# Performance work log

Hardware: AMD Instinct MI355X
Metric: run time of the kernel (lower is better)

The kernel has to match this reference:

```python
import jax, jax.numpy as jnp
import numpy as np

B, S, S2, H, NH, DF, NL, NLAYER = 512, 6, 32, 256, 8, 2048, 3, 3
HD = H // NH


def _layernorm(x, g, b, eps=1e-5):
    mu = x.mean(-1, keepdims=True)
    var = ((x - mu) ** 2).mean(-1, keepdims=True)
    return (x - mu) / jnp.sqrt(var + eps) * g + b


def _pos_encoding(seq, d):
    pos = jnp.arange(seq, dtype=jnp.float32)[:, None]
    div = jnp.exp(jnp.arange(0, d, 2, dtype=jnp.float32) * (-jnp.log(10000.0) / d))
    ang = pos * div  # [seq, d/2]
    return jnp.stack([jnp.sin(ang), jnp.cos(ang)], axis=-1).reshape(seq, d)


def setup_inputs() -> dict:
    key = jax.random.key(0)
    ks = iter(jax.random.split(key, 40))
    sc = 0.02
    inp = {}
    inp['states'] = jax.random.normal(next(ks), (B, S, H), jnp.float32)
    inp['state_mask'] = jax.random.randint(next(ks), (B, S), 0, 2).astype(jnp.float32)
    inp['actions'] = jax.random.normal(next(ks), (B, S2, H), jnp.float32)
    inp['actions_mask'] = jnp.ones((B, S2), jnp.float32)
    # TransformerEncoder params (3 layers, stacked on leading axis)
    inp['Wqkv'] = jax.random.normal(next(ks), (NLAYER, 3 * H, H), jnp.float32) * sc
    inp['bqkv'] = jnp.zeros((NLAYER, 3 * H), jnp.float32)
    inp['Wo'] = jax.random.normal(next(ks), (NLAYER, H, H), jnp.float32) * sc
    inp['bo'] = jnp.zeros((NLAYER, H), jnp.float32)
    inp['ln1_g'] = jnp.ones((NLAYER, H), jnp.float32)
    inp['ln1_b'] = jnp.zeros((NLAYER, H), jnp.float32)
    inp['W1'] = jax.random.normal(next(ks), (NLAYER, DF, H), jnp.float32) * sc
    inp['b1'] = jnp.zeros((NLAYER, DF), jnp.float32)
    inp['W2'] = jax.random.normal(next(ks), (NLAYER, H, DF), jnp.float32) * sc
    inp['b2'] = jnp.zeros((NLAYER, H), jnp.float32)
    inp['ln2_g'] = jnp.ones((NLAYER, H), jnp.float32)
    inp['ln2_b'] = jnp.zeros((NLAYER, H), jnp.float32)
    # attn_layer MLP: Linear(2H->H), ReLU, Linear(H->1), ReLU
    inp['Wa1'] = jax.random.normal(next(ks), (H, 2 * H), jnp.float32) * sc
    inp['ba1'] = jnp.zeros((H,), jnp.float32)
    inp['Wa2'] = jax.random.normal(next(ks), (1, H), jnp.float32) * sc
    inp['ba2'] = jnp.zeros((1,), jnp.float32)
    # dueling value head
    inp['Wv'] = jax.random.normal(next(ks), (1, H), jnp.float32) * sc
    inp['bv'] = jnp.zeros((1,), jnp.float32)
    # per-label bilinear weight [num_labels, H, H] + bias
    inp['Wlab'] = jax.random.normal(next(ks), (NL, H, H), jnp.float32) * sc
    inp['blab'] = jax.random.normal(next(ks), (NL,), jnp.float32) * sc
    return inp


def _forward(states, state_mask, actions, actions_mask, Wqkv, bqkv, Wo, bo,
             ln1_g, ln1_b, W1, b1, W2, b2, ln2_g, ln2_b,
             Wa1, ba1, Wa2, ba2, Wv, bv, Wlab, blab):
    batch, seq, hs = states.shape
    seq2 = actions.shape[1]
    # positional encoding along seq axis (eval mode: dropout = identity)
    x = states + _pos_encoding(seq, hs)[None, :, :]
    # Faithful to original: [batch, seq, h] is fed to a seq-first torch
    # TransformerEncoder, so self-attention mixes across the BATCH axis (L=batch,
    # N=seq). Post-LN layers, relu FFN, dim_feedforward=2048.
    for i in range(NLAYER):
        L, N = x.shape[0], x.shape[1]
        qkv = jnp.einsum('lne,fe->lnf', x, Wqkv[i]) + bqkv[i]
        q, k, v = jnp.split(qkv, 3, axis=-1)
        q = q.reshape(L, N, NH, HD)
        k = k.reshape(L, N, NH, HD)
        v = v.reshape(L, N, NH, HD)
        scores = jnp.einsum('lnhd,mnhd->nhlm', q, k) / jnp.sqrt(jnp.float32(HD))
        attn = jax.nn.softmax(scores, axis=-1)
        ctx = jnp.einsum('nhlm,mnhd->lnhd', attn, v).reshape(L, N, hs)
        sa = jnp.einsum('lne,fe->lnf', ctx, Wo[i]) + bo[i]
        x = _layernorm(x + sa, ln1_g[i], ln1_b[i])
        hmid = jax.nn.relu(jnp.einsum('lne,fe->lnf', x, W1[i]) + b1[i])
        ff = jnp.einsum('lnf,ef->lne', hmid, W2[i]) + b2[i]
        x = _layernorm(x + ff, ln2_g[i], ln2_b[i])
    out = x  # [batch, seq, h]
    # --- attention_aggregate(actions, out, out, actions_mask, state_mask) ---
    mask = actions_mask[:, :, None] * state_mask[:, None, :]  # [B, seq2, seq]
    stack = jnp.concatenate([
        jnp.broadcast_to(actions[:, :, None, :], (batch, seq2, seq, hs)),
        jnp.broadcast_to(out[:, None, :, :], (batch, seq2, seq, hs)),
    ], axis=-1)  # [B, seq2, seq, 2H]
    h1 = jax.nn.relu(jnp.einsum('bqkf,hf->bqkh', stack, Wa1) + ba1)
    a = jax.nn.relu(jnp.einsum('bqkh,oh->bqko', h1, Wa2)[..., 0] + ba2[0])
    A = jnp.where(mask > 0, jnp.exp(a), 0.0)  # masked_fill(-inf).exp()
    attn_w = A / jnp.clip(A.sum(-1, keepdims=True), 2e-15, None)
    states_feat = jnp.einsum('bqk,bkh->bqh', attn_w, out)  # [B, seq2, H]
    # -------------------------------------------------------------------
    actions_num = actions_mask.sum(1)[:, None, None]  # [B,1,1]
    states_feat_mean = states_feat.sum(1, keepdims=True) / actions_num  # [B,1,H]
    # adv[b,s,l] = sum_ij actions[b,s,i] * Wlab[l,i,j] * states_feat[b,s,j] + blab[l]
    adv = jnp.einsum('bsi,lij,bsj->bsl', actions, Wlab, states_feat) + blab
    val = states_feat_mean @ Wv.T + bv  # [B,1,1]
    q_value = val + adv - adv.mean(axis=(1, 2), keepdims=True)  # [B, seq2, NL]
    # actions_mask is all-ones -> no_pad selection keeps every row
    return q_value.reshape(-1, NL)


def reference(states, state_mask, actions, actions_mask, Wqkv, bqkv, Wo, bo,
              ln1_g, ln1_b, W1, b1, W2, b2, ln2_g, ln2_b,
              Wa1, ba1, Wa2, ba2, Wv, bv, Wlab, blab):
    return _forward(states, state_mask, actions, actions_mask, Wqkv, bqkv, Wo, bo,
                    ln1_g, ln1_b, W1, b1, W2, b2, ln2_g, ln2_b,
                    Wa1, ba1, Wa2, ba2, Wv, bv, Wlab, blab)
```

## Files before the change

kernel.cpp:

```cpp
#include <hip/hip_runtime.h>

using u16 = unsigned short;
typedef __attribute__((ext_vector_type(8))) short bf16x8;
typedef __attribute__((ext_vector_type(4))) float f32x4;

__device__ __forceinline__ float b2f(u16 u) { return __uint_as_float(((unsigned)u) << 16); }
__device__ __forceinline__ u16 f2b(float f) {
  unsigned x = __float_as_uint(f);
  return (u16)((x + 0x7FFFu + ((x >> 16) & 1u)) >> 16);
}

__device__ __align__(16) float g_xf[786432];
__device__ __align__(16) u16   g_xb[786432];
__device__ __align__(16) u16   g_qkv[2359296];
__device__ __align__(16) u16   g_ctx[786432];
__device__ __align__(16) u16   g_hmid[6291456];
__device__ __align__(16) u16   g_wb[3932160];
__device__ __align__(16) u16   g_actb[4194304];
__device__ __align__(16) u16   g_wa1b[131072];
__device__ __align__(16) u16   g_wlabb[196608];
__device__ __align__(16) float g_par[344584];
__device__ __align__(16) u16   g_Pab[4194304];
__device__ __align__(16) u16   g_Pob[786432];
__device__ __align__(16) u16   g_sfb[4194304];
__device__ float g_val[512];
__device__ float g_adv[49152];

#define OFF_BQKV 0
#define OFF_BO   2304
#define OFF_B1   3072
#define OFF_B2   9216
#define OFF_LN1G 9984
#define OFF_LN1B 10752
#define OFF_LN2G 11520
#define OFF_LN2B 12288
#define OFF_BA1  144128
#define OFF_WA2  144384
#define OFF_WV   144640
#define OFF_BLAB 341504
#define OFF_BA2  341508
#define OFF_BV   341509
#define OFF_MASK 341512

#define LP 40

__device__ __forceinline__ int get_flag(const unsigned* ln1g) {
  return (ln1g[0] == 0x3F800000u) ? 0 : 1;
}


struct PJob { const void* src; void* dst; void* dst2; int n; int kind; };
struct PJobs { PJob e[23]; };
__global__ __launch_bounds__(256) void prep_kernel(PJobs jobs, const unsigned* __restrict__ ln1g) {
  PJob j = jobs.e[blockIdx.y];
  int fl = get_flag(ln1g);
  int stride = gridDim.x * 256;
  int i0 = blockIdx.x * 256 + threadIdx.x;
  if (j.kind == 0) {
    float* dst = (float*)j.dst;
    for (int i = i0; i < j.n; i += stride)
      dst[i] = fl ? b2f(((const u16*)j.src)[i]) : ((const float*)j.src)[i];
  } else if (j.kind == 1) {
    int n8 = j.n >> 3;
    uint4* d = (uint4*)j.dst;
    if (fl) {
      const uint4* s = (const uint4*)j.src;
      for (int i = i0; i < n8; i += stride) d[i] = s[i];
    } else {
      const f32x4* s = (const f32x4*)j.src;
      for (int i = i0; i < n8; i += stride) {
        f32x4 v0 = s[i * 2];
        f32x4 v1 = s[i * 2 + 1];
        u16 tmp[8];
        #pragma unroll
        for (int k = 0; k < 4; k++) { tmp[k] = f2b(v0[k]); tmp[4 + k] = f2b(v1[k]); }
        d[i] = *(const uint4*)tmp;
      }
    }
  } else {
    float* xf = (float*)j.dst;
    u16* xb = (u16*)j.dst2;
    const float c = -9.210340371976184f / 256.f;
    for (int i = i0; i < j.n; i += stride) {
      size_t base = (size_t)i * 4;
      int t = (int)(base >> 8);
      int e = (int)(base & 255);
      int n = t % 6;
      int half = e >> 1;
      float dv0 = expf((float)(2 * half) * c);
      float dv1 = expf((float)(2 * (half + 1)) * c);
      float a0 = (float)n * dv0, a1 = (float)n * dv1;
      f32x4 p = { sinf(a0), cosf(a0), sinf(a1), cosf(a1) };
      f32x4 s;
      if (fl) {
        ushort4 u = *(const ushort4*)((const u16*)j.src + base);
        s[0] = b2f(u.x); s[1] = b2f(u.y); s[2] = b2f(u.z); s[3] = b2f(u.w);
      } else {
        s = *(const f32x4*)((const float*)j.src + base);
      }
      f32x4 v;
      #pragma unroll
      for (int k = 0; k < 4; k++) v[k] = s[k] + p[k];
      *(f32x4*)(xf + base) = v;
      ushort4 ob = { f2b(v[0]), f2b(v[1]), f2b(v[2]), f2b(v[3]) };
      *(ushort4*)(xb + base) = ob;
    }
  }
}

__device__ __forceinline__ float block_sum(float v, float* red) {
  int lane = threadIdx.x & 63;
  int w = threadIdx.x >> 6;
  #pragma unroll
  for (int o = 32; o > 0; o >>= 1) v += __shfl_down(v, o, 64);
  __syncthreads();
  if (lane == 0) red[w] = v;
  __syncthreads();
  int nw = blockDim.x >> 6;
  float s = 0.f;
  for (int i = 0; i < nw; i++) s += red[i];
  return s;
}

template <typename TC, bool RELU>
__global__ __launch_bounds__(256) void mfma_gemm(const u16* __restrict__ A,
                                                 const u16* __restrict__ B,
                                                 const float* __restrict__ bias,
                                                 TC* __restrict__ C,
                                                 int K, int lda, int ldb, int ldc) {
  __shared__ __align__(16) short As[64 * LP];
  __shared__ __align__(16) short Bs[64 * LP];
  int tx = threadIdx.x;
  int row0 = blockIdx.x * 64, col0 = blockIdx.y * 64;
  int lr = tx >> 2, lc = (tx & 3) * 8;
  int lane = tx & 63, w = tx >> 6;
  int wr = (w >> 1) * 32, wc = (w & 1) * 32;
  int q = lane >> 4, mr = lane & 15;
  f32x4 acc[2][2] = {};
  const short* Ap = (const short*)A;
  const short* Bp = (const short*)B;
  for (int k0 = 0; k0 < K; k0 += 32) {
    uint4 av = *(const uint4*)(Ap + (size_t)(row0 + lr) * lda + k0 + lc);
    uint4 bv = *(const uint4*)(Bp + (size_t)(col0 + lr) * ldb + k0 + lc);
    __syncthreads();
    *(uint4*)(As + lr * LP + lc) = av;
    *(uint4*)(Bs + lr * LP + lc) = bv;
    __syncthreads();
    bf16x8 af0 = *(const bf16x8*)(As + (wr + mr) * LP + q * 8);
    bf16x8 af1 = *(const bf16x8*)(As + (wr + 16 + mr) * LP + q * 8);
    bf16x8 bf0 = *(const bf16x8*)(Bs + (wc + mr) * LP + q * 8);
    bf16x8 bf1 = *(const bf16x8*)(Bs + (wc + 16 + mr) * LP + q * 8);
    acc[0][0] = __builtin_amdgcn_mfma_f32_16x16x32_bf16(af0, bf0, acc[0][0], 0, 0, 0);
    acc[0][1] = __builtin_amdgcn_mfma_f32_16x16x32_bf16(af0, bf1, acc[0][1], 0, 0, 0);
    acc[1][0] = __builtin_amdgcn_mfma_f32_16x16x32_bf16(af1, bf0, acc[1][0], 0, 0, 0);
    acc[1][1] = __builtin_amdgcn_mfma_f32_16x16x32_bf16(af1, bf1, acc[1][1], 0, 0, 0);
  }
  #pragma unroll
  for (int j = 0; j < 2; j++) {
    int col = col0 + wc + j * 16 + mr;
    float bv_ = bias ? bias[col] : 0.f;
    #pragma unroll
    for (int i = 0; i < 2; i++) {
      #pragma unroll
      for (int r = 0; r < 4; r++) {
        int row = row0 + wr + i * 16 + q * 4 + r;
        float v = acc[i][j][r] + bv_;
        if (RELU) v = fmaxf(v, 0.f);
        if constexpr (sizeof(TC) == 4) C[(size_t)row * ldc + col] = v;
        else C[(size_t)row * ldc + col] = f2b(v);
      }
    }
  }
}

template <typename TC, bool RELU>
__global__ __launch_bounds__(256) void mfma_gemm128(const u16* __restrict__ A,
                                                    const u16* __restrict__ B,
                                                    const float* __restrict__ bias,
                                                    TC* __restrict__ C,
                                                    int K, int lda, int ldb, int ldc) {
  __shared__ __align__(16) short As[128 * LP];
  __shared__ __align__(16) short Bs[128 * LP];
  int tx = threadIdx.x;
  int row0 = blockIdx.x * 128, col0 = blockIdx.y * 128;
  int lr = tx >> 2, lc = (tx & 3) * 8;
  int lane = tx & 63, w = tx >> 6;
  int wr = (w >> 1) * 64, wc = (w & 1) * 64;
  int q = lane >> 4, mr = lane & 15;
  f32x4 acc[4][4] = {};
  const short* Ap = (const short*)A;
  const short* Bp = (const short*)B;
  for (int k0 = 0; k0 < K; k0 += 32) {
    uint4 a0 = *(const uint4*)(Ap + (size_t)(row0 + lr) * lda + k0 + lc);
    uint4 a1 = *(const uint4*)(Ap + (size_t)(row0 + 64 + lr) * lda + k0 + lc);
    uint4 b0 = *(const uint4*)(Bp + (size_t)(col0 + lr) * ldb + k0 + lc);
    uint4 b1 = *(const uint4*)(Bp + (size_t)(col0 + 64 + lr) * ldb + k0 + lc);
    __syncthreads();
    *(uint4*)(As + lr * LP + lc) = a0;
    *(uint4*)(As + (64 + lr) * LP + lc) = a1;
    *(uint4*)(Bs + lr * LP + lc) = b0;
    *(uint4*)(Bs + (64 + lr) * LP + lc) = b1;
    __syncthreads();
    bf16x8 af[4], bf[4];
    #pragma unroll
    for (int i = 0; i < 4; i++) af[i] = *(const bf16x8*)(As + (wr + i * 16 + mr) * LP + q * 8);
    #pragma unroll
    for (int j = 0; j < 4; j++) bf[j] = *(const bf16x8*)(Bs + (wc + j * 16 + mr) * LP + q * 8);
    #pragma unroll
    for (int i = 0; i < 4; i++)
      #pragma unroll
      for (int j = 0; j < 4; j++)
        acc[i][j] = __builtin_amdgcn_mfma_f32_16x16x32_bf16(af[i], bf[j], acc[i][j], 0, 0, 0);
  }
  #pragma unroll
  for (int j = 0; j < 4; j++) {
    int col = col0 + wc + j * 16 + mr;
    float bv_ = bias ? bias[col] : 0.f;
    #pragma unroll
    for (int i = 0; i < 4; i++) {
      #pragma unroll
      for (int r = 0; r < 4; r++) {
        int row = row0 + wr + i * 16 + q * 4 + r;
        float v = acc[i][j][r] + bv_;
        if (RELU) v = fmaxf(v, 0.f);
        if constexpr (sizeof(TC) == 4) C[(size_t)row * ldc + col] = v;
        else C[(size_t)row * ldc + col] = f2b(v);
      }
    }
  }
}

__global__ __launch_bounds__(256) void papo_kernel(const u16* __restrict__ actb,
                                                   const u16* __restrict__ xb,
                                                   const u16* __restrict__ wa1b,
                                                   const float* __restrict__ ba1,
                                                   u16* __restrict__ Pab,
                                                   u16* __restrict__ Pob) {
  __shared__ __align__(16) short As[128 * LP];
  __shared__ __align__(16) short Bs[128 * LP];
  const short* Ap;
  const short* Bp;
  const float* bias;
  u16* C;
  int row0;
  if (blockIdx.x < 128) {
    Ap = (const short*)actb; Bp = (const short*)wa1b; bias = ba1; C = Pab;
    row0 = blockIdx.x * 128;
  } else {
    Ap = (const short*)xb; Bp = (const short*)(wa1b + 256); bias = nullptr; C = Pob;
    row0 = (blockIdx.x - 128) * 128;
  }
  const int K = 256, lda = 256, ldb = 512, ldc = 256;
  int tx = threadIdx.x;
  int col0 = blockIdx.y * 128;
  int lr = tx >> 2, lc = (tx & 3) * 8;
  int lane = tx & 63, w = tx >> 6;
  int wr = (w >> 1) * 64, wc = (w & 1) * 64;
  int q = lane >> 4, mr = lane & 15;
  f32x4 acc[4][4] = {};
  for (int k0 = 0; k0 < K; k0 += 32) {
    uint4 a0 = *(const uint4*)(Ap + (size_t)(row0 + lr) * lda + k0 + lc);
    uint4 a1 = *(const uint4*)(Ap + (size_t)(row0 + 64 + lr) * lda + k0 + lc);
    uint4 b0 = *(const uint4*)(Bp + (size_t)(col0 + lr) * ldb + k0 + lc);
    uint4 b1 = *(const uint4*)(Bp + (size_t)(col0 + 64 + lr) * ldb + k0 + lc);
    __syncthreads();
    *(uint4*)(As + lr * LP + lc) = a0;
    *(uint4*)(As + (64 + lr) * LP + lc) = a1;
    *(uint4*)(Bs + lr * LP + lc) = b0;
    *(uint4*)(Bs + (64 + lr) * LP + lc) = b1;
    __syncthreads();
    bf16x8 af[4], bf[4];
    #pragma unroll
    for (int i = 0; i < 4; i++) af[i] = *(const bf16x8*)(As + (wr + i * 16 + mr) * LP + q * 8);
    #pragma unroll
    for (int j = 0; j < 4; j++) bf[j] = *(const bf16x8*)(Bs + (wc + j * 16 + mr) * LP + q * 8);
    #pragma unroll
    for (int i = 0; i < 4; i++)
      #pragma unroll
      for (int j = 0; j < 4; j++)
        acc[i][j] = __builtin_amdgcn_mfma_f32_16x16x32_bf16(af[i], bf[j], acc[i][j], 0, 0, 0);
  }
  #pragma unroll
  for (int j = 0; j < 4; j++) {
    int col = col0 + wc + j * 16 + mr;
    float bv_ = bias ? bias[col] : 0.f;
    #pragma unroll
    for (int i = 0; i < 4; i++) {
      #pragma unroll
      for (int r = 0; r < 4; r++) {
        int row = row0 + wr + i * 16 + q * 4 + r;
        C[(size_t)row * ldc + col] = f2b(acc[i][j][r] + bv_);
      }
    }
  }
}

__global__ __launch_bounds__(256) void mfma_gemm_adv(const u16* __restrict__ A,
                                                     const u16* __restrict__ B,
                                                     const u16* __restrict__ actb,
                                                     float* __restrict__ adv,
                                                     int K, int lda, int ldb) {
  __shared__ __align__(16) short As[128 * LP];
  __shared__ __align__(16) short Bs[128 * LP];
  int tx = threadIdx.x;
  int row0 = blockIdx.x * 128, col0 = blockIdx.y * 128;
  int lr = tx >> 2, lc = (tx & 3) * 8;
  int lane = tx & 63, w = tx >> 6;
  int wr = (w >> 1) * 64, wc = (w & 1) * 64;
  int q = lane >> 4, mr = lane & 15;
  f32x4 acc[4][4] = {};
  const short* Ap = (const short*)A;
  const short* Bp = (const short*)B;
  for (int k0 = 0; k0 < K; k0 += 32) {
    uint4 a0 = *(const uint4*)(Ap + (size_t)(row0 + lr) * lda + k0 + lc);
    uint4 a1 = *(const uint4*)(Ap + (size_t)(row0 + 64 + lr) * lda + k0 + lc);
    uint4 b0 = *(const uint4*)(Bp + (size_t)(col0 + lr) * ldb + k0 + lc);
    uint4 b1 = *(const uint4*)(Bp + (size_t)(col0 + 64 + lr) * ldb + k0 + lc);
    __syncthreads();
    *(uint4*)(As + lr * LP + lc) = a0;
    *(uint4*)(As + (64 + lr) * LP + lc) = a1;
    *(uint4*)(Bs + lr * LP + lc) = b0;
    *(uint4*)(Bs + (64 + lr) * LP + lc) = b1;
    __syncthreads();
    bf16x8 af[4], bf[4];
    #pragma unroll
    for (int i = 0; i < 4; i++) af[i] = *(const bf16x8*)(As + (wr + i * 16 + mr) * LP + q * 8);
    #pragma unroll
    for (int j = 0; j < 4; j++) bf[j] = *(const bf16x8*)(Bs + (wc + j * 16 + mr) * LP + q * 8);
    #pragma unroll
    for (int i = 0; i < 4; i++)
      #pragma unroll
      for (int j = 0; j < 4; j++)
        acc[i][j] = __builtin_amdgcn_mfma_f32_16x16x32_bf16(af[i], bf[j], acc[i][j], 0, 0, 0);
  }
  int l = (col0 + wc) >> 8;
  #pragma unroll
  for (int i = 0; i < 4; i++) {
    #pragma unroll
    for (int r = 0; r < 4; r++) {
      int row = row0 + wr + i * 16 + q * 4 + r;
      float s = 0.f;
      #pragma unroll
      for (int j = 0; j < 4; j++) {
        int icol = (col0 + wc + j * 16 + mr) & 255;
        s += acc[i][j][r] * b2f(actb[(size_t)row * 256 + icol]);
      }
      s += __shfl_xor(s, 1, 64);
      s += __shfl_xor(s, 2, 64);
      s += __shfl_xor(s, 4, 64);
      s += __shfl_xor(s, 8, 64);
      if (mr == 0) atomicAdd(&adv[(size_t)row * 3 + l], s);
    }
  }
}

#define LP64 72
__global__ __launch_bounds__(256) void mfma_gemm_w2(const u16* __restrict__ A,
                                                    const u16* __restrict__ B,
                                                    const float* __restrict__ bias,
                                                    u16* __restrict__ C,
                                                    int K, int lda, int ldb, int ldc) {
  __shared__ __align__(16) short As[64 * LP64];
  __shared__ __align__(16) short Bs[32 * LP64];
  int tx = threadIdx.x;
  int row0 = blockIdx.x * 64, col0 = blockIdx.y * 32;
  int lane = tx & 63, w = tx >> 6;
  int wr = (w >> 1) * 32, wc = (w & 1) * 16;
  int q = lane >> 4, mr = lane & 15;
  int alr = tx >> 2, alc = (tx & 3) * 16;
  int blr = tx >> 3, blc = (tx & 7) * 8;
  f32x4 acc[2] = {};
  const short* Ap = (const short*)A;
  const short* Bp = (const short*)B;
  for (int k0 = 0; k0 < K; k0 += 64) {
    uint4 a0 = *(const uint4*)(Ap + (size_t)(row0 + alr) * lda + k0 + alc);
    uint4 a1 = *(const uint4*)(Ap + (size_t)(row0 + alr) * lda + k0 + alc + 8);
    uint4 b0 = *(const uint4*)(Bp + (size_t)(col0 + blr) * ldb + k0 + blc);
    __syncthreads();
    *(uint4*)(As + alr * LP64 + alc) = a0;
    *(uint4*)(As + alr * LP64 + alc + 8) = a1;
    *(uint4*)(Bs + blr * LP64 + blc) = b0;
    __syncthreads();
    #pragma unroll
    for (int kk = 0; kk < 64; kk += 32) {
      bf16x8 af0 = *(const bf16x8*)(As + (wr + mr) * LP64 + kk + q * 8);
      bf16x8 af1 = *(const bf16x8*)(As + (wr + 16 + mr) * LP64 + kk + q * 8);
      bf16x8 bf = *(const bf16x8*)(Bs + (wc + mr) * LP64 + kk + q * 8);
      acc[0] = __builtin_amdgcn_mfma_f32_16x16x32_bf16(af0, bf, acc[0], 0, 0, 0);
      acc[1] = __builtin_amdgcn_mfma_f32_16x16x32_bf16(af1, bf, acc[1], 0, 0, 0);
    }
  }
  int col = col0 + wc + mr;
  float bv_ = bias ? bias[col] : 0.f;
  #pragma unroll
  for (int i = 0; i < 2; i++) {
    #pragma unroll
    for (int r = 0; r < 4; r++) {
      int row = row0 + wr + i * 16 + q * 4 + r;
      C[(size_t)row * ldc + col] = f2b(acc[i][r] + bv_);
    }
  }
}

__global__ __launch_bounds__(256) void attn_mfma(const u16* __restrict__ qkv,
                                                 u16* __restrict__ ctx) {
  __shared__ __align__(16) u16 VT[32 * 72];
  __shared__ __align__(16) u16 Ss[64 * 72];
  int tx = threadIdx.x;
  int w = tx >> 6, lane = tx & 63;
  int q = lane >> 4, mr = lane & 15;
  int nh = blockIdx.x;
  int n = nh >> 3, h = nh & 7;
  int l0 = blockIdx.y * 64;
  int lrow = l0 + w * 16 + mr;
  bf16x8 af = *(const bf16x8*)(qkv + ((size_t)lrow * 6 + n) * 768 + h * 32 + q * 8);
  const float scale = 0.17677669529663687f;
  f32x4 acc_o[2] = {};
  float dpart[4] = {0.f, 0.f, 0.f, 0.f};
  for (int mi = 0; mi < 8; mi++) {
    int m0 = mi * 64;
    __syncthreads();
    {
      int row = tx >> 2;
      int dc = (tx & 3) * 8;
      uint4 vv = *(const uint4*)(qkv + ((size_t)(m0 + row) * 6 + n) * 768 + 512 + h * 32 + dc);
      u16 tmp[8];
      *(uint4*)tmp = vv;
      #pragma unroll
      for (int i = 0; i < 8; i++) VT[(dc + i) * 72 + row] = tmp[i];
    }
    f32x4 accs[4];
    #pragma unroll
    for (int nt = 0; nt < 4; nt++) {
      bf16x8 bf = *(const bf16x8*)(qkv + ((size_t)(m0 + nt * 16 + mr) * 6 + n) * 768 +
                                   256 + h * 32 + q * 8);
      f32x4 z = {0.f, 0.f, 0.f, 0.f};
      accs[nt] = __builtin_amdgcn_mfma_f32_16x16x32_bf16(af, bf, z, 0, 0, 0);
    }
    #pragma unroll
    for (int nt = 0; nt < 4; nt++) {
      #pragma unroll
      for (int r = 0; r < 4; r++) {
        float e = __expf(fminf(accs[nt][r] * scale, 60.f));
        dpart[r] += e;
        Ss[(w * 16 + q * 4 + r) * 72 + nt * 16 + mr] = f2b(e);
      }
    }
    __syncthreads();
    #pragma unroll
    for (int dt = 0; dt < 2; dt++) {
      #pragma unroll
      for (int kc = 0; kc < 2; kc++) {
        bf16x8 ap = *(const bf16x8*)(Ss + (w * 16 + mr) * 72 + kc * 32 + q * 8);
        bf16x8 bv = *(const bf16x8*)(VT + (dt * 16 + mr) * 72 + kc * 32 + q * 8);
        acc_o[dt] = __builtin_amdgcn_mfma_f32_16x16x32_bf16(ap, bv, acc_o[dt], 0, 0, 0);
      }
    }
  }
  #pragma unroll
  for (int r = 0; r < 4; r++) {
    float d = dpart[r];
    d += __shfl_xor(d, 1, 64);
    d += __shfl_xor(d, 2, 64);
    d += __shfl_xor(d, 4, 64);
    d += __shfl_xor(d, 8, 64);
    dpart[r] = d;
  }
  #pragma unroll
  for (int dt = 0; dt < 2; dt++) {
    #pragma unroll
    for (int r = 0; r < 4; r++) {
      int l = l0 + w * 16 + q * 4 + r;
      int d = dt * 16 + mr;
      ctx[((size_t)l * 6 + n) * 256 + h * 32 + d] = f2b(acc_o[dt][r] / dpart[r]);
    }
  }
}

__global__ __launch_bounds__(256) void ln_kernel(float* __restrict__ xf,
                                                 u16* __restrict__ xb,
                                                 const u16* __restrict__ addend,
                                                 const float* __restrict__ g,
                                                 const float* __restrict__ b) {
  int row = blockIdx.x * 4 + (threadIdx.x >> 6);
  int lane = threadIdx.x & 63;
  size_t base = (size_t)row * 256 + lane * 4;
  f32x4 x = *(const f32x4*)(xf + base);
  ushort4 ad = *(const ushort4*)(addend + base);
  f32x4 v;
  v[0] = x[0] + b2f(ad.x); v[1] = x[1] + b2f(ad.y);
  v[2] = x[2] + b2f(ad.z); v[3] = x[3] + b2f(ad.w);
  float s = (v[0] + v[1]) + (v[2] + v[3]);
  #pragma unroll
  for (int o = 32; o > 0; o >>= 1) s += __shfl_xor(s, o, 64);
  float mu = s * (1.f / 256.f);
  f32x4 d;
  #pragma unroll
  for (int j = 0; j < 4; j++) d[j] = v[j] - mu;
  float s2 = (d[0] * d[0] + d[1] * d[1]) + (d[2] * d[2] + d[3] * d[3]);
  #pragma unroll
  for (int o = 32; o > 0; o >>= 1) s2 += __shfl_xor(s2, o, 64);
  float rstd = 1.f / sqrtf(s2 * (1.f / 256.f) + 1e-5f);
  f32x4 gg = *(const f32x4*)(g + lane * 4);
  f32x4 bb = *(const f32x4*)(b + lane * 4);
  f32x4 y;
  #pragma unroll
  for (int j = 0; j < 4; j++) y[j] = d[j] * rstd * gg[j] + bb[j];
  *(f32x4*)(xf + base) = y;
  ushort4 ob = { f2b(y[0]), f2b(y[1]), f2b(y[2]), f2b(y[3]) };
  *(ushort4*)(xb + base) = ob;
}

#define PAP 260
__global__ __launch_bounds__(256) void agg_val_kernel(const u16* __restrict__ Pab,
                                                      const u16* __restrict__ Pob,
                                                      const float* __restrict__ Wa2,
                                                      const float* __restrict__ ba2,
                                                      const float* __restrict__ state_mask,
                                                      const float* __restrict__ out,
                                                      const float* __restrict__ Wv,
                                                      const float* __restrict__ bv,
                                                      u16* __restrict__ sfb,
                                                      float* __restrict__ val,
                                                      float* __restrict__ adv) {
  __shared__ __align__(16) float Pa_s[32 * PAP];
  __shared__ __align__(16) float Po_s[6 * PAP];
  __shared__ __align__(16) float out_s[6 * 256];
  __shared__ __align__(16) float wa2_s[256];
  __shared__ float Aw_s[192];
  __shared__ float inv_den_s[32];
  __shared__ float red[4];
  int b = blockIdx.x;
  int tx = threadIdx.x;
  if (tx < 96) adv[(size_t)b * 96 + tx] = 0.f;
  #pragma unroll
  for (int i = tx; i < 1024; i += 256) {
    int r = i >> 5, c8 = (i & 31) * 8;
    u16 vv[8];
    *(uint4*)vv = *(const uint4*)(Pab + ((size_t)(b * 32 + r) * 256 + c8));
    #pragma unroll
    for (int k = 0; k < 8; k++) Pa_s[r * PAP + c8 + k] = b2f(vv[k]);
  }
  if (tx < 192) {
    int r = tx >> 5, c8 = (tx & 31) * 8;
    u16 vv[8];
    *(uint4*)vv = *(const uint4*)(Pob + ((size_t)(b * 6 + r) * 256 + c8));
    #pragma unroll
    for (int k = 0; k < 8; k++) Po_s[r * PAP + c8 + k] = b2f(vv[k]);
  }
  for (int i = tx; i < 384; i += 256) {
    int e4 = i * 4;
    *(f32x4*)(out_s + e4) = *(const f32x4*)(out + (size_t)b * 1536 + e4);
  }
  if (tx < 64) *(f32x4*)(wa2_s + tx * 4) = *(const f32x4*)(Wa2 + tx * 4);
  __syncthreads();
  if (tx < 192) {
    int q = tx / 6, k = tx - q * 6;
    const float* paP = Pa_s + q * PAP;
    const float* poP = Po_s + k * PAP;
    float a0 = 0.f, a1 = 0.f, a2 = 0.f, a3 = 0.f;
    #pragma unroll 4
    for (int h = 0; h < 256; h += 4) {
      f32x4 pa = *(const f32x4*)(paP + h);
      f32x4 po = *(const f32x4*)(poP + h);
      f32x4 wv = *(const f32x4*)(wa2_s + h);
      a0 += fmaxf(pa[0] + po[0], 0.f) * wv[0];
      a1 += fmaxf(pa[1] + po[1], 0.f) * wv[1];
      a2 += fmaxf(pa[2] + po[2], 0.f) * wv[2];
      a3 += fmaxf(pa[3] + po[3], 0.f) * wv[3];
    }
    float s = (a0 + a1) + (a2 + a3) + ba2[0];
    float a = fminf(fmaxf(s, 0.f), 80.f);
    Aw_s[tx] = (state_mask[b * 6 + k] > 0.f) ? __expf(a) : 0.f;
  }
  __syncthreads();
  if (tx < 32) {
    const float* aw = Aw_s + tx * 6;
    float d = ((aw[0] + aw[1]) + (aw[2] + aw[3])) + (aw[4] + aw[5]);
    inv_den_s[tx] = 1.f / fmaxf(d, 2e-15f);
  }
  __syncthreads();
  float o0 = out_s[tx], o1 = out_s[256 + tx], o2 = out_s[512 + tx];
  float o3 = out_s[768 + tx], o4 = out_s[1024 + tx], o5 = out_s[1280 + tx];
  float msum = 0.f;
  #pragma unroll 4
  for (int q = 0; q < 32; q++) {
    const float* aw = Aw_s + q * 6;
    float acc = aw[0] * o0 + aw[1] * o1 + aw[2] * o2 + aw[3] * o3 + aw[4] * o4 + aw[5] * o5;
    float sfv = acc * inv_den_s[q];
    sfb[((size_t)(b * 32 + q)) * 256 + tx] = f2b(sfv);
    msum += sfv;
  }
  float vc = msum * (1.f / 32.f) * Wv[tx];
  float tot = block_sum(vc, red);
  if (tx == 0) val[b] = tot + bv[0];
}

__global__ __launch_bounds__(128) void final_kernel(const float* __restrict__ adv,
                                                    const float* __restrict__ blab,
                                                    const float* __restrict__ val,
                                                    void* __restrict__ out,
                                                    const unsigned* __restrict__ ln1g) {
  int b = blockIdx.x, t = threadIdx.x;
  __shared__ float red[2];
  float v = (t < 96) ? adv[(size_t)b * 96 + t] + blab[t % 3] : 0.f;
  float s = block_sum(v, red);
  float mean = s * (1.f / 96.f);
  if (t < 96) {
    float q = val[b] + v - mean;
    if (get_flag(ln1g)) ((u16*)out)[(size_t)b * 96 + t] = f2b(q);
    else                ((float*)out)[(size_t)b * 96 + t] = q;
  }
}

extern "C" void kernel_launch(void* const* d_in, const int* in_sizes, int n_in,
                              void* d_out, int out_size, void* d_ws, size_t ws_size,
                              hipStream_t stream) {
  float *xf, *par, *val, *adv;
  u16 *xb, *qkvb, *ctxb, *hmidb, *wb, *actb, *wa1b, *wlabb, *sfb, *Pab, *Pob;
  hipGetSymbolAddress((void**)&xf,    HIP_SYMBOL(g_xf));
  hipGetSymbolAddress((void**)&xb,    HIP_SYMBOL(g_xb));
  hipGetSymbolAddress((void**)&qkvb,  HIP_SYMBOL(g_qkv));
  hipGetSymbolAddress((void**)&ctxb,  HIP_SYMBOL(g_ctx));
  hipGetSymbolAddress((void**)&hmidb, HIP_SYMBOL(g_hmid));
  hipGetSymbolAddress((void**)&wb,    HIP_SYMBOL(g_wb));
  hipGetSymbolAddress((void**)&actb,  HIP_SYMBOL(g_actb));
  hipGetSymbolAddress((void**)&wa1b,  HIP_SYMBOL(g_wa1b));
  hipGetSymbolAddress((void**)&wlabb, HIP_SYMBOL(g_wlabb));
  hipGetSymbolAddress((void**)&par,   HIP_SYMBOL(g_par));
  hipGetSymbolAddress((void**)&Pab,   HIP_SYMBOL(g_Pab));
  hipGetSymbolAddress((void**)&Pob,   HIP_SYMBOL(g_Pob));
  hipGetSymbolAddress((void**)&sfb,   HIP_SYMBOL(g_sfb));
  hipGetSymbolAddress((void**)&val,   HIP_SYMBOL(g_val));
  hipGetSymbolAddress((void**)&adv,   HIP_SYMBOL(g_adv));
  const unsigned* ln1g = (const unsigned*)d_in[8];
  u16* sab = hmidb;
  u16* ffb = ctxb;

  PJobs pj;
  pj.e[0]  = { d_in[5],  par + OFF_BQKV, nullptr, 2304, 0 };
  pj.e[1]  = { d_in[7],  par + OFF_BO,   nullptr, 768,  0 };
  pj.e[2]  = { d_in[11], par + OFF_B1,   nullptr, 6144, 0 };
  pj.e[3]  = { d_in[13], par + OFF_B2,   nullptr, 768,  0 };
  pj.e[4]  = { d_in[8],  par + OFF_LN1G, nullptr, 768,  0 };
  pj.e[5]  = { d_in[9],  par + OFF_LN1B, nullptr, 768,  0 };
  pj.e[6]  = { d_in[14], par + OFF_LN2G, nullptr, 768,  0 };
  pj.e[7]  = { d_in[15], par + OFF_LN2B, nullptr, 768,  0 };
  pj.e[8]  = { d_in[17], par + OFF_BA1,  nullptr, 256,  0 };
  pj.e[9]  = { d_in[18], par + OFF_WA2,  nullptr, 256,  0 };
  pj.e[10] = { d_in[20], par + OFF_WV,   nullptr, 256,  0 };
  pj.e[11] = { d_in[23], par + OFF_BLAB, nullptr, 3,    0 };
  pj.e[12] = { d_in[19], par + OFF_BA2,  nullptr, 1,    0 };
  pj.e[13] = { d_in[21], par + OFF_BV,   nullptr, 1,    0 };
  pj.e[14] = { d_in[1],  par + OFF_MASK, nullptr, 3072, 0 };
  pj.e[15] = { d_in[4],  wb,             nullptr, 589824,  1 };
  pj.e[16] = { d_in[6],  wb + 589824,    nullptr, 196608,  1 };
  pj.e[17] = { d_in[10], wb + 786432,    nullptr, 1572864, 1 };
  pj.e[18] = { d_in[12], wb + 2359296,   nullptr, 1572864, 1 };
  pj.e[19] = { d_in[16], wa1b,           nullptr, 131072,  1 };
  pj.e[20] = { d_in[22], wlabb,          nullptr, 196608,  1 };
  pj.e[21] = { d_in[2],  actb,           nullptr, 4194304, 1 };
  pj.e[22] = { d_in[0],  xf,             xb,      196608,  2 };
  prep_kernel<<<dim3(128, 23), 256, 0, stream>>>(pj, ln1g);

  for (int i = 0; i < 3; i++) {
    mfma_gemm<u16, false><<<dim3(48, 12), 256, 0, stream>>>(
        xb, wb + (size_t)i * 196608, par + OFF_BQKV + i * 768, qkvb, 256, 256, 256, 768);
    attn_mfma<<<dim3(48, 8), 256, 0, stream>>>(qkvb, ctxb);
    mfma_gemm<u16, false><<<dim3(48, 4), 256, 0, stream>>>(
        ctxb, wb + 589824 + (size_t)i * 65536, par + OFF_BO + i * 256, sab, 256, 256, 256, 256);
    ln_kernel<<<768, 256, 0, stream>>>(xf, xb, sab, par + OFF_LN1G + i * 256, par + OFF_LN1B + i * 256);
    mfma_gemm128<u16, true><<<dim3(24, 16), 256, 0, stream>>>(
        xb, wb + 786432 + (size_t)i * 524288, par + OFF_B1 + i * 2048, hmidb, 256, 256, 256, 2048);
    mfma_gemm_w2<<<dim3(48, 8), 256, 0, stream>>>(
        hmidb, wb + 2359296 + (size_t)i * 524288, par + OFF_B2 + i * 256, ffb, 2048, 2048, 2048, 256);
    ln_kernel<<<768, 256, 0, stream>>>(xf, xb, ffb, par + OFF_LN2G + i * 256, par + OFF_LN2B + i * 256);
  }

  papo_kernel<<<dim3(152, 2), 256, 0, stream>>>(actb, xb, wa1b, par + OFF_BA1, Pab, Pob);

  agg_val_kernel<<<512, 256, 0, stream>>>(Pab, Pob, par + OFF_WA2, par + OFF_BA2,
                                          par + OFF_MASK, xf, par + OFF_WV,
                                          par + OFF_BV, sfb, val, adv);

  mfma_gemm_adv<<<dim3(128, 6), 256, 0, stream>>>(sfb, wlabb, actb, adv, 256, 256, 256);
  final_kernel<<<512, 128, 0, stream>>>(adv, par + OFF_BLAB, val, d_out, ln1g);
}
```

Baseline: 256.7 us.

## Stage full K=256 tiles in LDS once and shrink GEMM tiles to 64x64

The K=256 GEMMs (QKV, output projection, FFN1, attention-MLP projections, bilinear advantage) now load the whole 64x256 A and B tiles into shared memory in one pass. They then run all MFMA steps after a single barrier instead of looping over K in steps of 32 with two barriers per step. The former 128x128 kernels switch to 64x64 tiles with more blocks. The W2 GEMM widens its K step from 64 to 128. This removes barrier and global-latency stalls per K step and raises block counts, at the cost of about 66KB of LDS per block, which limits occupancy, and less operand reuse per block.

```diff
diff --git a/kernel.cpp b/kernel.cpp
--- a/kernel.cpp
+++ b/kernel.cpp
@@ -42,7 +42,8 @@
 #define OFF_BV   341509
 #define OFF_MASK 341512
 
-#define LP 40
+#define LPF 264
+#define LP128 136
 
 __device__ __forceinline__ int get_flag(const unsigned* ln1g) {
   return (ln1g[0] == 0x3F800000u) ? 0 : 1;
@@ -123,33 +124,40 @@
 }
 
 template <typename TC, bool RELU>
-__global__ __launch_bounds__(256) void mfma_gemm(const u16* __restrict__ A,
-                                                 const u16* __restrict__ B,
-                                                 const float* __restrict__ bias,
-                                                 TC* __restrict__ C,
-                                                 int K, int lda, int ldb, int ldc) {
-  __shared__ __align__(16) short As[64 * LP];
-  __shared__ __align__(16) short Bs[64 * LP];
+__global__ __launch_bounds__(256) void mfma_gemm_fs(const u16* __restrict__ A,
+                                                    const u16* __restrict__ B,
+                                                    const float* __restrict__ bias,
+                                                    TC* __restrict__ C,
+                                                    int lda, int ldb, int ldc) {
+  __shared__ __align__(16) short As[64 * LPF];
+  __shared__ __align__(16) short Bs[64 * LPF];
   int tx = threadIdx.x;
   int row0 = blockIdx.x * 64, col0 = blockIdx.y * 64;
-  int lr = tx >> 2, lc = (tx & 3) * 8;
+  int sr = tx >> 2, sc = (tx & 3) * 64;
   int lane = tx & 63, w = tx >> 6;
   int wr = (w >> 1) * 32, wc = (w & 1) * 32;
   int q = lane >> 4, mr = lane & 15;
-  f32x4 acc[2][2] = {};
   const short* Ap = (const short*)A;
   const short* Bp = (const short*)B;
-  for (int k0 = 0; k0 < K; k0 += 32) {
-    uint4 av = *(const uint4*)(Ap + (size_t)(row0 + lr) * lda + k0 + lc);
-    uint4 bv = *(const uint4*)(Bp + (size_t)(col0 + lr) * ldb + k0 + lc);
-    __syncthreads();
-    *(uint4*)(As + lr * LP + lc) = av;
-    *(uint4*)(Bs + lr * LP + lc) = bv;
-    __syncthreads();
-    bf16x8 af0 = *(const bf16x8*)(As + (wr + mr) * LP + q * 8);
-    bf16x8 af1 = *(const bf16x8*)(As + (wr + 16 + mr) * LP + q * 8);
-    bf16x8 bf0 = *(const bf16x8*)(Bs + (wc + mr) * LP + q * 8);
-    bf16x8 bf1 = *(const bf16x8*)(Bs + (wc + 16 + mr) * LP + q * 8);
+  uint4 ab[8], bb[8];
+  #pragma unroll
+  for (int c = 0; c < 8; c++)
+    ab[c] = *(const uint4*)(Ap + (size_t)(row0 + sr) * lda + sc + c * 8);
+  #pragma unroll
+  for (int c = 0; c < 8; c++)
+    bb[c] = *(const uint4*)(Bp + (size_t)(col0 + sr) * ldb + sc + c * 8);
+  #pragma unroll
+  for (int c = 0; c < 8; c++) *(uint4*)(As + sr * LPF + sc + c * 8) = ab[c];
+  #pragma unroll
+  for (int c = 0; c < 8; c++) *(uint4*)(Bs + sr * LPF + sc + c * 8) = bb[c];
+  __syncthreads();
+  f32x4 acc[2][2] = {};
+  #pragma unroll
+  for (int kk = 0; kk < 256; kk += 32) {
+    bf16x8 af0 = *(const bf16x8*)(As + (wr + mr) * LPF + kk + q * 8);
+    bf16x8 af1 = *(const bf16x8*)(As + (wr + 16 + mr) * LPF + kk + q * 8);
+    bf16x8 bf0 = *(const bf16x8*)(Bs + (wc + mr) * LPF + kk + q * 8);
+    bf16x8 bf1 = *(const bf16x8*)(Bs + (wc + 16 + mr) * LPF + kk + q * 8);
     acc[0][0] = __builtin_amdgcn_mfma_f32_16x16x32_bf16(af0, bf0, acc[0][0], 0, 0, 0);
     acc[0][1] = __builtin_amdgcn_mfma_f32_16x16x32_bf16(af0, bf1, acc[0][1], 0, 0, 0);
     acc[1][0] = __builtin_amdgcn_mfma_f32_16x16x32_bf16(af1, bf0, acc[1][0], 0, 0, 0);
@@ -173,119 +181,63 @@
   }
 }
 
-template <typename TC, bool RELU>
-__global__ __launch_bounds__(256) void mfma_gemm128(const u16* __restrict__ A,
-                                                    const u16* __restrict__ B,
-                                                    const float* __restrict__ bias,
-                                                    TC* __restrict__ C,
-                                                    int K, int lda, int ldb, int ldc) {
-  __shared__ __align__(16) short As[128 * LP];
-  __shared__ __align__(16) short Bs[128 * LP];
-  int tx = threadIdx.x;
-  int row0 = blockIdx.x * 128, col0 = blockIdx.y * 128;
-  int lr = tx >> 2, lc = (tx & 3) * 8;
-  int lane = tx & 63, w = tx >> 6;
-  int wr = (w >> 1) * 64, wc = (w & 1) * 64;
-  int q = lane >> 4, mr = lane & 15;
-  f32x4 acc[4][4] = {};
-  const short* Ap = (const short*)A;
-  const short* Bp = (const short*)B;
-  for (int k0 = 0; k0 < K; k0 += 32) {
-    uint4 a0 = *(const uint4*)(Ap + (size_t)(row0 + lr) * lda + k0 + lc);
-    uint4 a1 = *(const uint4*)(Ap + (size_t)(row0 + 64 + lr) * lda + k0 + lc);
-    uint4 b0 = *(const uint4*)(Bp + (size_t)(col0 + lr) * ldb + k0 + lc);
-    uint4 b1 = *(const uint4*)(Bp + (size_t)(col0 + 64 + lr) * ldb + k0 + lc);
-    __syncthreads();
-    *(uint4*)(As + lr * LP + lc) = a0;
-    *(uint4*)(As + (64 + lr) * LP + lc) = a1;
-    *(uint4*)(Bs + lr * LP + lc) = b0;
-    *(uint4*)(Bs + (64 + lr) * LP + lc) = b1;
-    __syncthreads();
-    bf16x8 af[4], bf[4];
-    #pragma unroll
-    for (int i = 0; i < 4; i++) af[i] = *(const bf16x8*)(As + (wr + i * 16 + mr) * LP + q * 8);
-    #pragma unroll
-    for (int j = 0; j < 4; j++) bf[j] = *(const bf16x8*)(Bs + (wc + j * 16 + mr) * LP + q * 8);
-    #pragma unroll
-    for (int i = 0; i < 4; i++)
-      #pragma unroll
-      for (int j = 0; j < 4; j++)
-        acc[i][j] = __builtin_amdgcn_mfma_f32_16x16x32_bf16(af[i], bf[j], acc[i][j], 0, 0, 0);
-  }
-  #pragma unroll
-  for (int j = 0; j < 4; j++) {
-    int col = col0 + wc + j * 16 + mr;
-    float bv_ = bias ? bias[col] : 0.f;
-    #pragma unroll
-    for (int i = 0; i < 4; i++) {
-      #pragma unroll
-      for (int r = 0; r < 4; r++) {
-        int row = row0 + wr + i * 16 + q * 4 + r;
-        float v = acc[i][j][r] + bv_;
-        if (RELU) v = fmaxf(v, 0.f);
-        if constexpr (sizeof(TC) == 4) C[(size_t)row * ldc + col] = v;
-        else C[(size_t)row * ldc + col] = f2b(v);
-      }
-    }
-  }
-}
-
-__global__ __launch_bounds__(256) void papo_kernel(const u16* __restrict__ actb,
-                                                   const u16* __restrict__ xb,
-                                                   const u16* __restrict__ wa1b,
-                                                   const float* __restrict__ ba1,
-                                                   u16* __restrict__ Pab,
-                                                   u16* __restrict__ Pob) {
-  __shared__ __align__(16) short As[128 * LP];
-  __shared__ __align__(16) short Bs[128 * LP];
+__global__ __launch_bounds__(256) void papo_fs(const u16* __restrict__ actb,
+                                               const u16* __restrict__ xb,
+                                               const u16* __restrict__ wa1b,
+                                               const float* __restrict__ ba1,
+                                               u16* __restrict__ Pab,
+                                               u16* __restrict__ Pob) {
+  __shared__ __align__(16) short As[64 * LPF];
+  __shared__ __align__(16) short Bs[64 * LPF];
   const short* Ap;
   const short* Bp;
   const float* bias;
   u16* C;
   int row0;
-  if (blockIdx.x < 128) {
+  if (blockIdx.x < 256) {
     Ap = (const short*)actb; Bp = (const short*)wa1b; bias = ba1; C = Pab;
-    row0 = blockIdx.x * 128;
+    row0 = blockIdx.x * 64;
   } else {
     Ap = (const short*)xb; Bp = (const short*)(wa1b + 256); bias = nullptr; C = Pob;
-    row0 = (blockIdx.x - 128) * 128;
-  }
-  const int K = 256, lda = 256, ldb = 512, ldc = 256;
+    row0 = (blockIdx.x - 256) * 64;
+  }
+  const int lda = 256, ldb = 512, ldc = 256;
   int tx = threadIdx.x;
-  int col0 = blockIdx.y * 128;
-  int lr = tx >> 2, lc = (tx & 3) * 8;
+  int col0 = blockIdx.y * 64;
+  int sr = tx >> 2, sc = (tx & 3) * 64;
   int lane = tx & 63, w = tx >> 6;
-  int wr = (w >> 1) * 64, wc = (w & 1) * 64;
+  int wr = (w >> 1) * 32, wc = (w & 1) * 32;
   int q = lane >> 4, mr = lane & 15;
-  f32x4 acc[4][4] = {};
-  for (int k0 = 0; k0 < K; k0 += 32) {
-    uint4 a0 = *(const uint4*)(Ap + (size_t)(row0 + lr) * lda + k0 + lc);
-    uint4 a1 = *(const uint4*)(Ap + (size_t)(row0 + 64 + lr) * lda + k0 + lc);
-    uint4 b0 = *(const uint4*)(Bp + (size_t)(col0 + lr) * ldb + k0 + lc);
-    uint4 b1 = *(const uint4*)(Bp + (size_t)(col0 + 64 + lr) * ldb + k0 + lc);
-    __syncthreads();
-    *(uint4*)(As + lr * LP + lc) = a0;
-    *(uint4*)(As + (64 + lr) * LP + lc) = a1;
-    *(uint4*)(Bs + lr * LP + lc) = b0;
-    *(uint4*)(Bs + (64 + lr) * LP + lc) = b1;
-    __syncthreads();
-    bf16x8 af[4], bf[4];
-    #pragma unroll
-    for (int i = 0; i < 4; i++) af[i] = *(const bf16x8*)(As + (wr + i * 16 + mr) * LP + q * 8);
-    #pragma unroll
-    for (int j = 0; j < 4; j++) bf[j] = *(const bf16x8*)(Bs + (wc + j * 16 + mr) * LP + q * 8);
-    #pragma unroll
-    for (int i = 0; i < 4; i++)
-      #pragma unroll
-      for (int j = 0; j < 4; j++)
-        acc[i][j] = __builtin_amdgcn_mfma_f32_16x16x32_bf16(af[i], bf[j], acc[i][j], 0, 0, 0);
-  }
-  #pragma unroll
-  for (int j = 0; j < 4; j++) {
+  uint4 ab[8], bb[8];
+  #pragma unroll
+  for (int c = 0; c < 8; c++)
+    ab[c] = *(const uint4*)(Ap + (size_t)(row0 + sr) * lda + sc + c * 8);
+  #pragma unroll
+  for (int c = 0; c < 8; c++)
+    bb[c] = *(const uint4*)(Bp + (size_t)(col0 + sr) * ldb + sc + c * 8);
+  #pragma unroll
+  for (int c = 0; c < 8; c++) *(uint4*)(As + sr * LPF + sc + c * 8) = ab[c];
+  #pragma unroll
+  for (int c = 0; c < 8; c++) *(uint4*)(Bs + sr * LPF + sc + c * 8) = bb[c];
+  __syncthreads();
+  f32x4 acc[2][2] = {};
+  #pragma unroll
+  for (int kk = 0; kk < 256; kk += 32) {
+    bf16x8 af0 = *(const bf16x8*)(As + (wr + mr) * LPF + kk + q * 8);
+    bf16x8 af1 = *(const bf16x8*)(As + (wr + 16 + mr) * LPF + kk + q * 8);
+    bf16x8 bf0 = *(const bf16x8*)(Bs + (wc + mr) * LPF + kk + q * 8);
+    bf16x8 bf1 = *(const bf16x8*)(Bs + (wc + 16 + mr) * LPF + kk + q * 8);
+    acc[0][0] = __builtin_amdgcn_mfma_f32_16x16x32_bf16(af0, bf0, acc[0][0], 0, 0, 0);
+    acc[0][1] = __builtin_amdgcn_mfma_f32_16x16x32_bf16(af0, bf1, acc[0][1], 0, 0, 0);
+    acc[1][0] = __builtin_amdgcn_mfma_f32_16x16x32_bf16(af1, bf0, acc[1][0], 0, 0, 0);
+    acc[1][1] = __builtin_amdgcn_mfma_f32_16x16x32_bf16(af1, bf1, acc[1][1], 0, 0, 0);
+  }
+  #pragma unroll
+  for (int j = 0; j < 2; j++) {
     int col = col0 + wc + j * 16 + mr;
     float bv_ = bias ? bias[col] : 0.f;
     #pragma unroll
-    for (int i = 0; i < 4; i++) {
+    for (int i = 0; i < 2; i++) {
       #pragma unroll
       for (int r = 0; r < 4; r++) {
         int row = row0 + wr + i * 16 + q * 4 + r;
@@ -295,53 +247,54 @@
   }
 }
 
-__global__ __launch_bounds__(256) void mfma_gemm_adv(const u16* __restrict__ A,
-                                                     const u16* __restrict__ B,
-                                                     const u16* __restrict__ actb,
-                                                     float* __restrict__ adv,
-                                                     int K, int lda, int ldb) {
-  __shared__ __align__(16) short As[128 * LP];
-  __shared__ __align__(16) short Bs[128 * LP];
+__global__ __launch_bounds__(256) void adv_fs(const u16* __restrict__ A,
+                                              const u16* __restrict__ B,
+                                              const u16* __restrict__ actb,
+                                              float* __restrict__ adv) {
+  __shared__ __align__(16) short As[64 * LPF];
+  __shared__ __align__(16) short Bs[64 * LPF];
+  const int lda = 256, ldb = 256;
   int tx = threadIdx.x;
-  int row0 = blockIdx.x * 128, col0 = blockIdx.y * 128;
-  int lr = tx >> 2, lc = (tx & 3) * 8;
+  int row0 = blockIdx.x * 64, col0 = blockIdx.y * 64;
+  int sr = tx >> 2, sc = (tx & 3) * 64;
   int lane = tx & 63, w = tx >> 6;
-  int wr = (w >> 1) * 64, wc = (w & 1) * 64;
+  int wr = (w >> 1) * 32, wc = (w & 1) * 32;
   int q = lane >> 4, mr = lane & 15;
-  f32x4 acc[4][4] = {};
   const short* Ap = (const short*)A;
   const short* Bp = (const short*)B;
-  for (int k0 = 0; k0 < K; k0 += 32) {
-    uint4 a0 = *(const uint4*)(Ap + (size_t)(row0 + lr) * lda + k0 + lc);
-    uint4 a1 = *(const uint4*)(Ap + (size_t)(row0 + 64 + lr) * lda + k0 + lc);
-    uint4 b0 = *(const uint4*)(Bp + (size_t)(col0 + lr) * ldb + k0 + lc);
-    uint4 b1 = *(const uint4*)(Bp + (size_t)(col0 + 64 + lr) * ldb + k0 + lc);
-    __syncthreads();
-    *(uint4*)(As + lr * LP + lc) = a0;
-    *(uint4*)(As + (64 + lr) * LP + lc) = a1;
-    *(uint4*)(Bs + lr * LP + lc) = b0;
-    *(uint4*)(Bs + (64 + lr) * LP + lc) = b1;
-    __syncthreads();
-    bf16x8 af[4], bf[4];
-    #pragma unroll
-    for (int i = 0; i < 4; i++) af[i] = *(const bf16x8*)(As + (wr + i * 16 + mr) * LP + q * 8);
-    #pragma unroll
-    for (int j = 0; j < 4; j++) bf[j] = *(const bf16x8*)(Bs + (wc + j * 16 + mr) * LP + q * 8);
-    #pragma unroll
-    for (int i = 0; i < 4; i++)
-      #pragma unroll
-      for (int j = 0; j < 4; j++)
-        acc[i][j] = __builtin_amdgcn_mfma_f32_16x16x32_bf16(af[i], bf[j], acc[i][j], 0, 0, 0);
-  }
-  int l = (col0 + wc) >> 8;
-  #pragma unroll
-  for (int i = 0; i < 4; i++) {
+  uint4 ab[8], bb[8];
+  #pragma unroll
+  for (int c = 0; c < 8; c++)
+    ab[c] = *(const uint4*)(Ap + (size_t)(row0 + sr) * lda + sc + c * 8);
+  #pragma unroll
+  for (int c = 0; c < 8; c++)
+    bb[c] = *(const uint4*)(Bp + (size_t)(col0 + sr) * ldb + sc + c * 8);
+  #pragma unroll
+  for (int c = 0; c < 8; c++) *(uint4*)(As + sr * LPF + sc + c * 8) = ab[c];
+  #pragma unroll
+  for (int c = 0; c < 8; c++) *(uint4*)(Bs + sr * LPF + sc + c * 8) = bb[c];
+  __syncthreads();
+  f32x4 acc[2][2] = {};
+  #pragma unroll
+  for (int kk = 0; kk < 256; kk += 32) {
+    bf16x8 af0 = *(const bf16x8*)(As + (wr + mr) * LPF + kk + q * 8);
+    bf16x8 af1 = *(const bf16x8*)(As + (wr + 16 + mr) * LPF + kk + q * 8);
+    bf16x8 bf0 = *(const bf16x8*)(Bs + (wc + mr) * LPF + kk + q * 8);
+    bf16x8 bf1 = *(const bf16x8*)(Bs + (wc + 16 + mr) * LPF + kk + q * 8);
+    acc[0][0] = __builtin_amdgcn_mfma_f32_16x16x32_bf16(af0, bf0, acc[0][0], 0, 0, 0);
+    acc[0][1] = __builtin_amdgcn_mfma_f32_16x16x32_bf16(af0, bf1, acc[0][1], 0, 0, 0);
+    acc[1][0] = __builtin_amdgcn_mfma_f32_16x16x32_bf16(af1, bf0, acc[1][0], 0, 0, 0);
+    acc[1][1] = __builtin_amdgcn_mfma_f32_16x16x32_bf16(af1, bf1, acc[1][1], 0, 0, 0);
+  }
+  int l = col0 >> 8;
+  #pragma unroll
+  for (int i = 0; i < 2; i++) {
     #pragma unroll
     for (int r = 0; r < 4; r++) {
       int row = row0 + wr + i * 16 + q * 4 + r;
       float s = 0.f;
       #pragma unroll
-      for (int j = 0; j < 4; j++) {
+      for (int j = 0; j < 2; j++) {
         int icol = (col0 + wc + j * 16 + mr) & 255;
         s += acc[i][j][r] * b2f(actb[(size_t)row * 256 + icol]);
       }
@@ -354,38 +307,43 @@
   }
 }
 
-#define LP64 72
 __global__ __launch_bounds__(256) void mfma_gemm_w2(const u16* __restrict__ A,
                                                     const u16* __restrict__ B,
                                                     const float* __restrict__ bias,
                                                     u16* __restrict__ C,
                                                     int K, int lda, int ldb, int ldc) {
-  __shared__ __align__(16) short As[64 * LP64];
-  __shared__ __align__(16) short Bs[32 * LP64];
+  __shared__ __align__(16) short As[64 * LP128];
+  __shared__ __align__(16) short Bs[32 * LP128];
   int tx = threadIdx.x;
   int row0 = blockIdx.x * 64, col0 = blockIdx.y * 32;
   int lane = tx & 63, w = tx >> 6;
   int wr = (w >> 1) * 32, wc = (w & 1) * 16;
   int q = lane >> 4, mr = lane & 15;
-  int alr = tx >> 2, alc = (tx & 3) * 16;
-  int blr = tx >> 3, blc = (tx & 7) * 8;
+  int alr = tx >> 2, alc = (tx & 3) * 32;
+  int blr = tx >> 3, blc = (tx & 7) * 16;
   f32x4 acc[2] = {};
   const short* Ap = (const short*)A;
   const short* Bp = (const short*)B;
-  for (int k0 = 0; k0 < K; k0 += 64) {
+  for (int k0 = 0; k0 < K; k0 += 128) {
     uint4 a0 = *(const uint4*)(Ap + (size_t)(row0 + alr) * lda + k0 + alc);
     uint4 a1 = *(const uint4*)(Ap + (size_t)(row0 + alr) * lda + k0 + alc + 8);
+    uint4 a2 = *(const uint4*)(Ap + (size_t)(row0 + alr) * lda + k0 + alc + 16);
+    uint4 a3 = *(const uint4*)(Ap + (size_t)(row0 + alr) * lda + k0 + alc + 24);
     uint4 b0 = *(const uint4*)(Bp + (size_t)(col0 + blr) * ldb + k0 + blc);
+    uint4 b1 = *(const uint4*)(Bp + (size_t)(col0 + blr) * ldb + k0 + blc + 8);
     __syncthreads();
-    *(uint4*)(As + alr * LP64 + alc) = a0;
-    *(uint4*)(As + alr * LP64 + alc + 8) = a1;
-    *(uint4*)(Bs + blr * LP64 + blc) = b0;
+    *(uint4*)(As + alr * LP128 + alc) = a0;
+    *(uint4*)(As + alr * LP128 + alc + 8) = a1;
+    *(uint4*)(As + alr * LP128 + alc + 16) = a2;
+    *(uint4*)(As + alr * LP128 + alc + 24) = a3;
+    *(uint4*)(Bs + blr * LP128 + blc) = b0;
+    *(uint4*)(Bs + blr * LP128 + blc + 8) = b1;
     __syncthreads();
     #pragma unroll
-    for (int kk = 0; kk < 64; kk += 32) {
-      bf16x8 af0 = *(const bf16x8*)(As + (wr + mr) * LP64 + kk + q * 8);
-      bf16x8 af1 = *(const bf16x8*)(As + (wr + 16 + mr) * LP64 + kk + q * 8);
-      bf16x8 bf = *(const bf16x8*)(Bs + (wc + mr) * LP64 + kk + q * 8);
+    for (int kk = 0; kk < 128; kk += 32) {
+      bf16x8 af0 = *(const bf16x8*)(As + (wr + mr) * LP128 + kk + q * 8);
+      bf16x8 af1 = *(const bf16x8*)(As + (wr + 16 + mr) * LP128 + kk + q * 8);
+      bf16x8 bf = *(const bf16x8*)(Bs + (wc + mr) * LP128 + kk + q * 8);
       acc[0] = __builtin_amdgcn_mfma_f32_16x16x32_bf16(af0, bf, acc[0], 0, 0, 0);
       acc[1] = __builtin_amdgcn_mfma_f32_16x16x32_bf16(af1, bf, acc[1], 0, 0, 0);
     }
@@ -664,25 +622,25 @@
   prep_kernel<<<dim3(128, 23), 256, 0, stream>>>(pj, ln1g);
 
   for (int i = 0; i < 3; i++) {
-    mfma_gemm<u16, false><<<dim3(48, 12), 256, 0, stream>>>(
-        xb, wb + (size_t)i * 196608, par + OFF_BQKV + i * 768, qkvb, 256, 256, 256, 768);
+    mfma_gemm_fs<u16, false><<<dim3(48, 12), 256, 0, stream>>>(
+        xb, wb + (size_t)i * 196608, par + OFF_BQKV + i * 768, qkvb, 256, 256, 768);
     attn_mfma<<<dim3(48, 8), 256, 0, stream>>>(qkvb, ctxb);
-    mfma_gemm<u16, false><<<dim3(48, 4), 256, 0, stream>>>(
-        ctxb, wb + 589824 + (size_t)i * 65536, par + OFF_BO + i * 256, sab, 256, 256, 256, 256);
+    mfma_gemm_fs<u16, false><<<dim3(48, 4), 256, 0, stream>>>(
+        ctxb, wb + 589824 + (size_t)i * 65536, par + OFF_BO + i * 256, sab, 256, 256, 256);
     ln_kernel<<<768, 256, 0, stream>>>(xf, xb, sab, par + OFF_LN1G + i * 256, par + OFF_LN1B + i * 256);
-    mfma_gemm128<u16, true><<<dim3(24, 16), 256, 0, stream>>>(
-        xb, wb + 786432 + (size_t)i * 524288, par + OFF_B1 + i * 2048, hmidb, 256, 256, 256, 2048);
+    mfma_gemm_fs<u16, true><<<dim3(48, 32), 256, 0, stream>>>(
+        xb, wb + 786432 + (size_t)i * 524288, par + OFF_B1 + i * 2048, hmidb, 256, 256, 2048);
     mfma_gemm_w2<<<dim3(48, 8), 256, 0, stream>>>(
         hmidb, wb + 2359296 + (size_t)i * 524288, par + OFF_B2 + i * 256, ffb, 2048, 2048, 2048, 256);
     ln_kernel<<<768, 256, 0, stream>>>(xf, xb, ffb, par + OFF_LN2G + i * 256, par + OFF_LN2B + i * 256);
   }
 
-  papo_kernel<<<dim3(152, 2), 256, 0, stream>>>(actb, xb, wa1b, par + OFF_BA1, Pab, Pob);
+  papo_fs<<<dim3(304, 4), 256, 0, stream>>>(actb, xb, wa1b, par + OFF_BA1, Pab, Pob);
 
   agg_val_kernel<<<512, 256, 0, stream>>>(Pab, Pob, par + OFF_WA2, par + OFF_BA2,
                                           par + OFF_MASK, xf, par + OFF_WV,
                                           par + OFF_BV, sfb, val, adv);
 
-  mfma_gemm_adv<<<dim3(128, 6), 256, 0, stream>>>(sfb, wlabb, actb, adv, 256, 256, 256);
+  adv_fs<<<dim3(256, 12), 256, 0, stream>>>(sfb, wlabb, actb, adv);
   final_kernel<<<512, 128, 0, stream>>>(adv, par + OFF_BLAB, val, d_out, ln1g);
 }
```

Result: slower. 304.4 us (+18.6%).
